# Kernel optimization log

Measured on AMD Instinct MI355X. Metric: run time of the kernel, lower is better.

Reference implementation:

```python
import jax, jax.numpy as jnp
import numpy as np

D_MODEL = 1024
N_HEADS = 16
DH = D_MODEL // N_HEADS
ROPE_THETA = 10000.0


def rotate_half(u):
    h = u.shape[-1] // 2
    return jnp.concatenate([-u[..., h:], u[..., :h]], axis=-1)


def apply_rope(q, k, cos, sin):
    return q * cos + rotate_half(q) * sin, k * cos + rotate_half(k) * sin


def setup_inputs() -> dict:
    key = jax.random.key(0)
    ks = jax.random.split(key, 6)
    B, S = 2, 2048
    x = jax.random.normal(ks[0], (B, S, D_MODEL), dtype=jnp.float32)
    y = jax.random.normal(ks[1], (B, S, D_MODEL), dtype=jnp.float32)
    wq = 0.01 * jax.random.normal(ks[2], (D_MODEL, D_MODEL), dtype=jnp.float32)
    wk = 0.01 * jax.random.normal(ks[3], (D_MODEL, D_MODEL), dtype=jnp.float32)
    wv = 0.01 * jax.random.normal(ks[4], (D_MODEL, D_MODEL), dtype=jnp.float32)
    wo = 0.01 * jax.random.normal(ks[5], (D_MODEL, D_MODEL), dtype=jnp.float32)
    return {"x": x, "y": y, "wq": wq, "wk": wk, "wv": wv, "wo": wo}


def reference(x, y, wq, wk, wv, wo):
    B, S, D = x.shape
    past_length = 0  # default; kv_cache=None

    Q = x @ wq.T                      # (B,S,D)
    K = y                             # NOTE: K is y un-projected (as in source)
    V = y @ wv.T
    # K1 = x @ wk.T is computed in the source but immediately overwritten
    # by the buggy second apply_rope call -> wk is unused in the output.
    V1 = x @ wo.T

    def heads(t):
        return t.reshape(B, S, N_HEADS, DH).transpose(0, 2, 1, 3)  # (B,H,S,dh)

    q_h, k_h, v_h, v1_h = heads(Q), heads(K), heads(V), heads(V1)

    # RoPE tables (past_length:past_length+S rows of the cache)
    freqs = 1.0 / ROPE_THETA ** (jnp.arange(0, DH, 2, dtype=jnp.float32) / DH)
    emb = jnp.arange(past_length, past_length + S, dtype=jnp.float32)[:, None] * freqs[None, :]
    cos = jnp.concatenate([jnp.cos(emb), jnp.cos(emb)], axis=-1)[None, None]  # (1,1,S,dh)
    sin = jnp.concatenate([jnp.sin(emb), jnp.sin(emb)], axis=-1)[None, None]

    q_h, k_h = apply_rope(q_h, k_h, cos, sin)
    # faithful to source: k1 = rope applied AGAIN to the already-roped k
    _, k1_h = apply_rope(q_h, k_h, cos, sin)

    k_full = jnp.concatenate([k_h, k1_h], axis=2)   # (B,H,2S,dh)
    v_full = jnp.concatenate([v_h, v1_h], axis=2)
    S_full = k_full.shape[2]

    # mask: tril(diagonal=past_length) over (S,S_full), last S cols = eye(S)
    rows = jnp.arange(S)[:, None]
    cols = jnp.arange(S_full)[None, :]
    mask = cols <= rows + past_length
    mask = mask.at[:, -S:].set(jnp.eye(S, dtype=bool))  # (S,S_full)

    scores = jnp.einsum("bhqd,bhkd->bhqk", q_h, k_full) / jnp.sqrt(jnp.asarray(DH, x.dtype))
    scores = jnp.where(mask[None, None], scores, jnp.asarray(-1e30, x.dtype))
    attn = jax.nn.softmax(scores, axis=-1)
    out = jnp.einsum("bhqk,bhkd->bhqd", attn, v_full)
    out = out.transpose(0, 2, 1, 3).reshape(B, S, D)

    k_ret = k_full[:, :, :-S, :]
    return out, k_ret
```

## Files before the change

kernel.cpp:

```cpp
#include <hip/hip_runtime.h>

#define DM 1024
#define NHEADS 16
#define DHEAD 64
#define BB 2
#define SS 2048
#define BH (BB*NHEADS)

typedef __attribute__((ext_vector_type(8))) short short8;
typedef __attribute__((ext_vector_type(4))) float float4v;
typedef unsigned short ushort_t;

#define LN1E4_D32 0.28782313662425572f

static __device__ __forceinline__ unsigned short f2bf(float f) {
    union { float f; unsigned u; } v; v.f = f;
    unsigned r = v.u + 0x7fffu + ((v.u >> 16) & 1u);
    return (unsigned short)(r >> 16);
}
static __device__ __forceinline__ float bf2f(unsigned short u) {
    union { float f; unsigned u; } v; v.u = ((unsigned)u) << 16;
    return v.f;
}

static __device__ __forceinline__ void gload16(const ushort_t* g, ushort_t* l) {
    __builtin_amdgcn_global_load_lds(
        (const __attribute__((address_space(1))) void*)g,
        (__attribute__((address_space(3))) void*)l, 16, 0, 0);
}

__global__ __launch_bounds__(256) void cvt_tile_kernel(
        const float* __restrict__ x, const float* __restrict__ wq,
        const float* __restrict__ wv, const float* __restrict__ wo,
        ushort_t* __restrict__ xb, ushort_t* __restrict__ wqb,
        ushort_t* __restrict__ wvb, ushort_t* __restrict__ wob) {
    int C = blockIdx.x * 256 + threadIdx.x;
    int c  = C & 511;
    int tl = C >> 9;
    int rb = tl >> 5, kb = tl & 31;
    const float* src; ushort_t* dst; int r0;
    if (rb < 32)      { src = x;  r0 = rb * 128;        dst = xb  + (size_t)tl * 4096; }
    else if (rb < 40) { src = wq; r0 = (rb - 32) * 128; dst = wqb + (size_t)(((rb - 32) * 32) + kb) * 4096; }
    else if (rb < 48) { src = wv; r0 = (rb - 40) * 128; dst = wvb + (size_t)(((rb - 40) * 32) + kb) * 4096; }
    else              { src = wo; r0 = (rb - 48) * 128; dst = wob + (size_t)(((rb - 48) * 32) + kb) * 4096; }
    int row = c >> 2, g = c & 3;
    int kk3 = g ^ ((row >> 1) & 3);
    const float* s = src + (size_t)(r0 + row) * DM + kb * 32 + kk3 * 8;
    float4 a0 = *reinterpret_cast<const float4*>(s);
    float4 a1 = *reinterpret_cast<const float4*>(s + 4);
    short8 v;
    v[0] = (short)f2bf(a0.x); v[1] = (short)f2bf(a0.y);
    v[2] = (short)f2bf(a0.z); v[3] = (short)f2bf(a0.w);
    v[4] = (short)f2bf(a1.x); v[5] = (short)f2bf(a1.y);
    v[6] = (short)f2bf(a1.z); v[7] = (short)f2bf(a1.w);
    *reinterpret_cast<short8*>(dst + c * 8) = v;
}

__global__ __launch_bounds__(256) void rope_k_kernel(const float* __restrict__ y,
        float* __restrict__ kout, ushort_t* __restrict__ khb, ushort_t* __restrict__ yb) {
    int t = blockIdx.x * blockDim.x + threadIdx.x;
    int i8 = t & 3;
    int s  = (t >> 2) & (SS - 1);
    int bh = t >> 13;
    int h = bh & (NHEADS - 1), b = bh >> 4;

    const float* yp = y + ((size_t)(b * SS + s)) * DM + h * DHEAD + i8 * 8;
    float4 a0 = *reinterpret_cast<const float4*>(yp);
    float4 a1 = *reinterpret_cast<const float4*>(yp + 4);
    float4 b0 = *reinterpret_cast<const float4*>(yp + 32);
    float4 b1 = *reinterpret_cast<const float4*>(yp + 36);
    float u0[8] = {a0.x, a0.y, a0.z, a0.w, a1.x, a1.y, a1.z, a1.w};
    float u1[8] = {b0.x, b0.y, b0.z, b0.w, b1.x, b1.y, b1.z, b1.w};
    float lo[8], hi[8];
#pragma unroll
    for (int j = 0; j < 8; j++) {
        int i = i8 * 8 + j;
        float freq = __expf(-(float)i * LN1E4_D32);
        float th = (float)s * freq;
        float cv = cosf(th), sv = sinf(th);
        lo[j] = u0[j] * cv - u1[j] * sv;
        hi[j] = u1[j] * cv + u0[j] * sv;
    }
    float* op = kout + ((size_t)bh * SS + s) * DHEAD + i8 * 8;
    *reinterpret_cast<float4*>(op)      = (float4){lo[0], lo[1], lo[2], lo[3]};
    *reinterpret_cast<float4*>(op + 4)  = (float4){lo[4], lo[5], lo[6], lo[7]};
    *reinterpret_cast<float4*>(op + 32) = (float4){hi[0], hi[1], hi[2], hi[3]};
    *reinterpret_cast<float4*>(op + 36) = (float4){hi[4], hi[5], hi[6], hi[7]};

    ushort_t* kb = khb + ((size_t)bh * 32 + (s >> 6)) * 4096 + (s & 63) * 64;
    short8 vlo, vhi;
#pragma unroll
    for (int j = 0; j < 8; j++) { vlo[j] = (short)f2bf(lo[j]); vhi[j] = (short)f2bf(hi[j]); }
    *reinterpret_cast<short8*>(kb + ((i8 ^ (s & 7)) << 3))       = vlo;
    *reinterpret_cast<short8*>(kb + (((i8 + 4) ^ (s & 7)) << 3)) = vhi;

    int rowm = b * SS + s;
    int rowin = rowm & 127, rbm = rowm >> 7;
    int g = i8 ^ ((rowin >> 1) & 3);
    ushort_t* yt = yb + ((size_t)(rbm * 32 + h * 2)) * 4096 + rowin * 32 + (g << 3);
    short8 ulo, uhi;
#pragma unroll
    for (int j = 0; j < 8; j++) { ulo[j] = (short)f2bf(u0[j]); uhi[j] = (short)f2bf(u1[j]); }
    *reinterpret_cast<short8*>(yt)        = ulo;
    *reinterpret_cast<short8*>(yt + 4096) = uhi;
}

__global__ __launch_bounds__(256, 2) void gemm3_kernel(
        const ushort_t* __restrict__ xb, const ushort_t* __restrict__ yb,
        const ushort_t* __restrict__ wqb, const ushort_t* __restrict__ wvb,
        const ushort_t* __restrict__ wob,
        ushort_t* __restrict__ qh, ushort_t* __restrict__ vt, ushort_t* __restrict__ v1h) {
    __shared__ __align__(16) char smem[34816];
    ushort_t* As = (ushort_t*)smem;
    ushort_t* Bs = (ushort_t*)(smem + 16384);
    ushort_t (*Ct)[136] = (ushort_t(*)[136])smem;

    int bid = blockIdx.x;
    int xcd = bid & 7;
    int s_  = bid >> 3;
    int zo  = s_ >> 5;
    int z   = (zo == 0) ? 0 : (zo == 1 ? 2 : 1);
    int t_  = s_ & 31;
    int n0  = (t_ >> 2) * 128;
    int m0  = (xcd * 4 + (t_ & 3)) * 128;

    const ushort_t* A = (z == 1) ? yb : xb;
    const ushort_t* W = (z == 0) ? wqb : (z == 1 ? wvb : wob);
    ushort_t* O = (z == 0) ? qh : (z == 1 ? vt : v1h);

    const ushort_t* Atl = A + (size_t)(m0 >> 7) * 32 * 4096;
    const ushort_t* Wtl = W + (size_t)(n0 >> 7) * 32 * 4096;

    int tid = threadIdx.x;
    int wave = tid >> 6, lane = tid & 63, quad = lane >> 4, l15 = lane & 15;
    int wr = (wave >> 1) * 64, wc = (wave & 1) * 64;

    int gi0 = tid * 8, gi1 = (256 + tid) * 8;
    int li0 = (tid & 192) * 8, li1 = (256 + (tid & 192)) * 8;

    int aoff[4], boff[4];
#pragma unroll
    for (int mi = 0; mi < 4; mi++) {
        int row = wr + mi * 16 + l15;
        aoff[mi] = row * 32 + ((quad ^ ((row >> 1) & 3)) << 3);
    }
#pragma unroll
    for (int ni = 0; ni < 4; ni++) {
        int row = wc + ni * 16 + l15;
        boff[ni] = row * 32 + ((quad ^ ((row >> 1) & 3)) << 3);
    }

    float4v acc[4][4];
#pragma unroll
    for (int a = 0; a < 4; a++)
#pragma unroll
        for (int b = 0; b < 4; b++)
            acc[a][b] = (float4v){0.f, 0.f, 0.f, 0.f};

    gload16(Atl + gi0, As + li0); gload16(Atl + gi1, As + li1);
    gload16(Wtl + gi0, Bs + li0); gload16(Wtl + gi1, Bs + li1);
    int cur = 0;

    for (int kb = 0; kb < 32; kb++) {
        __syncthreads();
        if (kb + 1 < 32) {
            const ushort_t* at = Atl + (size_t)(kb + 1) * 4096;
            const ushort_t* wt = Wtl + (size_t)(kb + 1) * 4096;
            int nb = (cur ^ 1) * 4096;
            gload16(at + gi0, As + nb + li0); gload16(at + gi1, As + nb + li1);
            gload16(wt + gi0, Bs + nb + li0); gload16(wt + gi1, Bs + nb + li1);
        }
        const ushort_t* Ac = As + cur * 4096;
        const ushort_t* Bc = Bs + cur * 4096;
        short8 af[4], bfr[4];
#pragma unroll
        for (int mi = 0; mi < 4; mi++)
            af[mi] = *reinterpret_cast<const short8*>(&Ac[aoff[mi]]);
#pragma unroll
        for (int ni = 0; ni < 4; ni++)
            bfr[ni] = *reinterpret_cast<const short8*>(&Bc[boff[ni]]);
#pragma unroll
        for (int mi = 0; mi < 4; mi++)
#pragma unroll
            for (int ni = 0; ni < 4; ni++)
                acc[mi][ni] = __builtin_amdgcn_mfma_f32_16x16x32_bf16(af[mi], bfr[ni], acc[mi][ni], 0, 0, 0);
        cur ^= 1;
    }

    if (z == 0) {
#pragma unroll
        for (int mi = 0; mi < 4; mi++)
#pragma unroll
            for (int r = 0; r < 4; r++) {
                int m = m0 + wr + mi * 16 + quad * 4 + r;
                float pos = (float)(m & (SS - 1));
#pragma unroll
                for (int ni = 0; ni < 2; ni++) {
                    int d = ni * 16 + l15;
                    float f = __expf(-(float)d * LN1E4_D32);
                    float th = pos * f;
                    float cv, sv;
                    __sincosf(th, &sv, &cv);
                    float u0 = acc[mi][ni][r], u1 = acc[mi][ni + 2][r];
                    acc[mi][ni][r]     = u0 * cv - u1 * sv;
                    acc[mi][ni + 2][r] = u1 * cv + u0 * sv;
                }
            }
    }

    __syncthreads();
#pragma unroll
    for (int mi = 0; mi < 4; mi++)
#pragma unroll
        for (int ni = 0; ni < 4; ni++) {
            int col = wc + ni * 16 + l15;
#pragma unroll
            for (int r = 0; r < 4; r++)
                Ct[wr + mi * 16 + quad * 4 + r][col] = f2bf(acc[mi][ni][r]);
        }
    __syncthreads();
    int h0 = n0 >> 6;
    if (z == 1) {
        int b = m0 >> 11;
        int s0 = m0 & (SS - 1);
#pragma unroll
        for (int it = 0; it < 8; it++) {
            int c = it * 256 + tid;
            int dh  = c & 63;
            int k16 = (c >> 6) & 15;
            int hh  = c >> 10;
            short8 v;
#pragma unroll
            for (int e = 0; e < 8; e++)
                v[e] = (short)Ct[k16 * 8 + e][hh * 64 + dh];
            int kt = (s0 >> 6) + (k16 >> 3);
            size_t off = ((size_t)((b * NHEADS + h0 + hh) * 32 + kt)) * 4096
                       + dh * 64 + (((k16 & 7) ^ (dh & 7)) << 3);
            *reinterpret_cast<short8*>(&O[off]) = v;
        }
    } else {
#pragma unroll
        for (int it = 0; it < 8; it++) {
            int c = it * 256 + tid;
            int o = c >> 3, j = c & 7;
            int hh = o >> 7, mr = o & 127;
            int m = m0 + mr, b = m >> 11, si = m & (SS - 1);
            uint4 v = *reinterpret_cast<const uint4*>(&Ct[mr][hh * 64 + j * 8]);
            *reinterpret_cast<uint4*>(
                &O[((size_t)((b * NHEADS + h0 + hh) * SS + si)) * DHEAD + j * 8]) = v;
        }
    }
}

__global__ __launch_bounds__(256, 2) void attn_kernel(
        const ushort_t* __restrict__ qh, const float* __restrict__ kf32,
        const ushort_t* __restrict__ khb, const ushort_t* __restrict__ vtb,
        const ushort_t* __restrict__ v1h, float* __restrict__ out) {
    __shared__ __align__(16) ushort_t Ks[2][4096];
    __shared__ __align__(16) ushort_t Vt[2][4096];
    __shared__ ushort_t Ps[4][16][68];
    __shared__ float sdiag[4][16];

    int bid = blockIdx.x;
    int bh = (bid & 7) * 4 + ((bid >> 3) & 3);
    int qb = 31 - (bid >> 5);
    int q0 = qb * 64;

    int tid = threadIdx.x, wave = tid >> 6, lane = tid & 63, quad = lane >> 4, l15 = lane & 15;
    int q0w = q0 + wave * 16;
    const ushort_t* qp  = qh  + (size_t)bh * SS * DHEAD;
    const float*    kp  = kf32 + (size_t)bh * SS * DHEAD;
    const ushort_t* v1p = v1h + (size_t)bh * SS * DHEAD;
    const ushort_t* ktb = khb + (size_t)bh * 32 * 4096;
    const ushort_t* vtt = vtb + (size_t)bh * 32 * 4096;

    short8 qf[2];
    qf[0] = *reinterpret_cast<const short8*>(&qp[(q0w + l15) * DHEAD + quad * 8]);
    qf[1] = *reinterpret_cast<const short8*>(&qp[(q0w + l15) * DHEAD + 32 + quad * 8]);

    float4v Oa[4];
#pragma unroll
    for (int t = 0; t < 4; t++) Oa[t] = (float4v){0.f, 0.f, 0.f, 0.f};
    float lsum[4] = {0.f, 0.f, 0.f, 0.f};

    int gi0 = tid * 8, gi1 = (256 + tid) * 8;
    int li0 = (tid & 192) * 8, li1 = (256 + (tid & 192)) * 8;

    int ntiles = qb + 1;
    gload16(ktb + gi0, &Ks[0][li0]); gload16(ktb + gi1, &Ks[0][li1]);
    gload16(vtt + gi0, &Vt[0][li0]); gload16(vtt + gi1, &Vt[0][li1]);
    int cur = 0;

    for (int kt = 0; kt < ntiles; kt++) {
        __syncthreads();
        if (kt + 1 < ntiles) {
            const ushort_t* gk = ktb + (size_t)(kt + 1) * 4096;
            const ushort_t* gv = vtt + (size_t)(kt + 1) * 4096;
            int nb = cur ^ 1;
            gload16(gk + gi0, &Ks[nb][li0]); gload16(gk + gi1, &Ks[nb][li1]);
            gload16(gv + gi0, &Vt[nb][li0]); gload16(gv + gi1, &Vt[nb][li1]);
        }
        const ushort_t* Kc = Ks[cur];
        const ushort_t* Vc = Vt[cur];

        float4v sa[4];
#pragma unroll
        for (int t2 = 0; t2 < 4; t2++) sa[t2] = (float4v){0.f, 0.f, 0.f, 0.f};
#pragma unroll
        for (int t2 = 0; t2 < 4; t2++) {
            int key = t2 * 16 + l15;
            int ro = key * 64, sw = key & 7;
#pragma unroll
            for (int half = 0; half < 2; half++) {
                short8 kf = *reinterpret_cast<const short8*>(&Kc[ro + (((half * 4 + quad) ^ sw) << 3)]);
                sa[t2] = __builtin_amdgcn_mfma_f32_16x16x32_bf16(qf[half], kf, sa[t2], 0, 0, 0);
            }
        }

        int kbase = kt * 64;
#pragma unroll
        for (int r = 0; r < 4; r++) {
            int query = q0w + quad * 4 + r;
#pragma unroll
            for (int t2 = 0; t2 < 4; t2++) {
                int key = kbase + t2 * 16 + l15;
                float p = (key <= query) ? __expf(sa[t2][r] * 0.125f) : 0.f;
                Ps[wave][quad * 4 + r][t2 * 16 + l15] = f2bf(p);
                lsum[r] += p;
            }
        }
        short8 pf0 = *reinterpret_cast<const short8*>(&Ps[wave][l15][quad * 8]);
        short8 pf1 = *reinterpret_cast<const short8*>(&Ps[wave][l15][32 + quad * 8]);
#pragma unroll
        for (int t = 0; t < 4; t++) {
            int dh = t * 16 + l15;
            int ro = dh * 64, sw = dh & 7;
            short8 vf0 = *reinterpret_cast<const short8*>(&Vc[ro + ((quad ^ sw) << 3)]);
            short8 vf1 = *reinterpret_cast<const short8*>(&Vc[ro + (((4 + quad) ^ sw) << 3)]);
            Oa[t] = __builtin_amdgcn_mfma_f32_16x16x32_bf16(pf0, vf0, Oa[t], 0, 0, 0);
            Oa[t] = __builtin_amdgcn_mfma_f32_16x16x32_bf16(pf1, vf1, Oa[t], 0, 0, 0);
        }
        cur ^= 1;
    }

    {
        int sk = q0w + l15;
        const float* krow = kp + (size_t)sk * DHEAD;
        short8 k1lo, k1hi;
#pragma unroll
        for (int j = 0; j < 8; j++) {
            int d = quad * 8 + j;
            float f = __expf(-(float)d * LN1E4_D32);
            float th = (float)sk * f;
            float cv, sv;
            __sincosf(th, &sv, &cv);
            float a = krow[d], b2 = krow[d + 32];
            k1lo[j] = (short)f2bf(a * cv - b2 * sv);
            k1hi[j] = (short)f2bf(b2 * cv + a * sv);
        }
        float4v sd4 = (float4v){0.f, 0.f, 0.f, 0.f};
        sd4 = __builtin_amdgcn_mfma_f32_16x16x32_bf16(qf[0], k1lo, sd4, 0, 0, 0);
        sd4 = __builtin_amdgcn_mfma_f32_16x16x32_bf16(qf[1], k1hi, sd4, 0, 0, 0);
#pragma unroll
        for (int r = 0; r < 4; r++)
            if (l15 == quad * 4 + r) sdiag[wave][l15] = sd4[r] * 0.125f;
        __syncthreads();

        int b = bh >> 4, h = bh & (NHEADS - 1);
#pragma unroll
        for (int r = 0; r < 4; r++) {
            float ls = lsum[r];
#pragma unroll
            for (int off = 1; off < 16; off <<= 1) ls += __shfl_xor(ls, off);
            float pd = __expf(sdiag[wave][quad * 4 + r]);
            int query = q0w + quad * 4 + r;
            float linv = 1.f / (ls + pd);
#pragma unroll
            for (int t = 0; t < 4; t++) {
                float v1v = bf2f(v1p[query * DHEAD + t * 16 + l15]);
                float o = (Oa[t][r] + pd * v1v) * linv;
                out[(b * SS + query) * DM + h * DHEAD + t * 16 + l15] = o;
            }
        }
    }
}

extern "C" void kernel_launch(void* const* d_in, const int* in_sizes, int n_in,
                              void* d_out, int out_size, void* d_ws, size_t ws_size,
                              hipStream_t stream) {
    const float* x  = (const float*)d_in[0];
    const float* y  = (const float*)d_in[1];
    const float* wq = (const float*)d_in[2];
    const float* wv = (const float*)d_in[4];
    const float* wo = (const float*)d_in[5];
    float* outp  = (float*)d_out;
    float* k_out = outp + (size_t)BB * SS * DM;

    char* ws = (char*)d_ws;
    ushort_t* vtb = (ushort_t*)(ws);
    ushort_t* v1b = (ushort_t*)(ws + (8ull  << 20));
    ushort_t* qhb = (ushort_t*)(ws + (16ull << 20));
    ushort_t* khb = (ushort_t*)(ws + (24ull << 20));
    ushort_t* xb  = (ushort_t*)(ws + (32ull << 20));
    ushort_t* yb  = (ushort_t*)(ws + (40ull << 20));
    ushort_t* wqb = (ushort_t*)(ws + (48ull << 20));
    ushort_t* wvb = (ushort_t*)(ws + (50ull << 20));
    ushort_t* wob = (ushort_t*)(ws + (52ull << 20));

    cvt_tile_kernel<<<3584, 256, 0, stream>>>(x, wq, wv, wo, xb, wqb, wvb, wob);
    rope_k_kernel<<<1024, 256, 0, stream>>>(y, k_out, khb, yb);
    gemm3_kernel<<<768, 256, 0, stream>>>(xb, yb, wqb, wvb, wob, qhb, vtb, v1b);
    attn_kernel<<<1024, 256, 0, stream>>>(qhb, k_out, khb, vtb, v1b, outp);
}
```

Before: 184.6 us.

## Peel masked diagonal tile and transpose QK MFMA for packed P stores

Splits the key loop so all off-diagonal tiles run a mask-free path and only the final diagonal tile applies the causal mask. It also swaps the MFMA operand order so each lane holds four consecutive keys for one query, which allows packed bf16 conversion and 32-bit stores into the P scratch (padded to 70). The row-sum reduction becomes two cross-quad shuffles plus a shared-memory exchange instead of per-row 16-lane butterflies. The intent is to cut VALU and LDS work in the inner loop, at the cost of an extra shared array and using inline assembly for the conversion.

```diff
diff --git a/kernel.cpp b/kernel.cpp
--- a/kernel.cpp
+++ b/kernel.cpp
@@ -21,6 +21,11 @@
 static __device__ __forceinline__ float bf2f(unsigned short u) {
     union { float f; unsigned u; } v; v.u = ((unsigned)u) << 16;
     return v.f;
+}
+static __device__ __forceinline__ unsigned cvtpk_bf16(float lo, float hi) {
+    unsigned r;
+    asm("v_cvt_pk_bf16_f32 %0, %1, %2" : "=v"(r) : "v"(lo), "v"(hi));
+    return r;
 }
 
 static __device__ __forceinline__ void gload16(const ushort_t* g, ushort_t* l) {
@@ -252,14 +257,66 @@
     }
 }
 
+template<bool MASKED>
+static __device__ __forceinline__ void attn_tile(
+        const ushort_t* __restrict__ Kc, const ushort_t* __restrict__ Vc, int kbase,
+        int quad, int l15, int q0w, const short8* qf,
+        ushort_t (*Psw)[70], float4v* Oa, float& lsum) {
+    float4v sa[4];
+#pragma unroll
+    for (int t2 = 0; t2 < 4; t2++) sa[t2] = (float4v){0.f, 0.f, 0.f, 0.f};
+#pragma unroll
+    for (int t2 = 0; t2 < 4; t2++) {
+        int key = t2 * 16 + l15;
+        int ro = key * 64, sw = key & 7;
+#pragma unroll
+        for (int half = 0; half < 2; half++) {
+            short8 kf = *reinterpret_cast<const short8*>(&Kc[ro + (((half * 4 + quad) ^ sw) << 3)]);
+            sa[t2] = __builtin_amdgcn_mfma_f32_16x16x32_bf16(kf, qf[half], sa[t2], 0, 0, 0);
+        }
+    }
+    int query = q0w + l15;
+#pragma unroll
+    for (int t2 = 0; t2 < 4; t2++) {
+        float p[4];
+#pragma unroll
+        for (int r = 0; r < 4; r++) {
+            float e = __expf(sa[t2][r] * 0.125f);
+            if (MASKED) {
+                int key = kbase + t2 * 16 + quad * 4 + r;
+                p[r] = (key <= query) ? e : 0.f;
+            } else {
+                p[r] = e;
+            }
+        }
+        lsum += (p[0] + p[1]) + (p[2] + p[3]);
+        unsigned w0 = cvtpk_bf16(p[0], p[1]);
+        unsigned w1 = cvtpk_bf16(p[2], p[3]);
+        *reinterpret_cast<unsigned*>(&Psw[l15][t2 * 16 + quad * 4])     = w0;
+        *reinterpret_cast<unsigned*>(&Psw[l15][t2 * 16 + quad * 4 + 2]) = w1;
+    }
+    short8 pf0 = *reinterpret_cast<const short8*>(&Psw[l15][quad * 8]);
+    short8 pf1 = *reinterpret_cast<const short8*>(&Psw[l15][32 + quad * 8]);
+#pragma unroll
+    for (int t = 0; t < 4; t++) {
+        int dh = t * 16 + l15;
+        int ro = dh * 64, sw = dh & 7;
+        short8 vf0 = *reinterpret_cast<const short8*>(&Vc[ro + ((quad ^ sw) << 3)]);
+        short8 vf1 = *reinterpret_cast<const short8*>(&Vc[ro + (((4 + quad) ^ sw) << 3)]);
+        Oa[t] = __builtin_amdgcn_mfma_f32_16x16x32_bf16(pf0, vf0, Oa[t], 0, 0, 0);
+        Oa[t] = __builtin_amdgcn_mfma_f32_16x16x32_bf16(pf1, vf1, Oa[t], 0, 0, 0);
+    }
+}
+
 __global__ __launch_bounds__(256, 2) void attn_kernel(
         const ushort_t* __restrict__ qh, const float* __restrict__ kf32,
         const ushort_t* __restrict__ khb, const ushort_t* __restrict__ vtb,
         const ushort_t* __restrict__ v1h, float* __restrict__ out) {
     __shared__ __align__(16) ushort_t Ks[2][4096];
     __shared__ __align__(16) ushort_t Vt[2][4096];
-    __shared__ ushort_t Ps[4][16][68];
+    __shared__ ushort_t Ps[4][16][70];
     __shared__ float sdiag[4][16];
+    __shared__ float sred[4][16];
 
     int bid = blockIdx.x;
     int bh = (bid & 7) * 4 + ((bid >> 3) & 3);
@@ -281,67 +338,31 @@
     float4v Oa[4];
 #pragma unroll
     for (int t = 0; t < 4; t++) Oa[t] = (float4v){0.f, 0.f, 0.f, 0.f};
-    float lsum[4] = {0.f, 0.f, 0.f, 0.f};
+    float lsum = 0.f;
 
     int gi0 = tid * 8, gi1 = (256 + tid) * 8;
     int li0 = (tid & 192) * 8, li1 = (256 + (tid & 192)) * 8;
 
-    int ntiles = qb + 1;
     gload16(ktb + gi0, &Ks[0][li0]); gload16(ktb + gi1, &Ks[0][li1]);
     gload16(vtt + gi0, &Vt[0][li0]); gload16(vtt + gi1, &Vt[0][li1]);
     int cur = 0;
 
-    for (int kt = 0; kt < ntiles; kt++) {
+    for (int kt = 0; kt < qb; kt++) {
         __syncthreads();
-        if (kt + 1 < ntiles) {
-            const ushort_t* gk = ktb + (size_t)(kt + 1) * 4096;
-            const ushort_t* gv = vtt + (size_t)(kt + 1) * 4096;
-            int nb = cur ^ 1;
-            gload16(gk + gi0, &Ks[nb][li0]); gload16(gk + gi1, &Ks[nb][li1]);
-            gload16(gv + gi0, &Vt[nb][li0]); gload16(gv + gi1, &Vt[nb][li1]);
-        }
-        const ushort_t* Kc = Ks[cur];
-        const ushort_t* Vc = Vt[cur];
-
-        float4v sa[4];
-#pragma unroll
-        for (int t2 = 0; t2 < 4; t2++) sa[t2] = (float4v){0.f, 0.f, 0.f, 0.f};
-#pragma unroll
-        for (int t2 = 0; t2 < 4; t2++) {
-            int key = t2 * 16 + l15;
-            int ro = key * 64, sw = key & 7;
-#pragma unroll
-            for (int half = 0; half < 2; half++) {
-                short8 kf = *reinterpret_cast<const short8*>(&Kc[ro + (((half * 4 + quad) ^ sw) << 3)]);
-                sa[t2] = __builtin_amdgcn_mfma_f32_16x16x32_bf16(qf[half], kf, sa[t2], 0, 0, 0);
-            }
-        }
-
-        int kbase = kt * 64;
-#pragma unroll
-        for (int r = 0; r < 4; r++) {
-            int query = q0w + quad * 4 + r;
-#pragma unroll
-            for (int t2 = 0; t2 < 4; t2++) {
-                int key = kbase + t2 * 16 + l15;
-                float p = (key <= query) ? __expf(sa[t2][r] * 0.125f) : 0.f;
-                Ps[wave][quad * 4 + r][t2 * 16 + l15] = f2bf(p);
-                lsum[r] += p;
-            }
-        }
-        short8 pf0 = *reinterpret_cast<const short8*>(&Ps[wave][l15][quad * 8]);
-        short8 pf1 = *reinterpret_cast<const short8*>(&Ps[wave][l15][32 + quad * 8]);
-#pragma unroll
-        for (int t = 0; t < 4; t++) {
-            int dh = t * 16 + l15;
-            int ro = dh * 64, sw = dh & 7;
-            short8 vf0 = *reinterpret_cast<const short8*>(&Vc[ro + ((quad ^ sw) << 3)]);
-            short8 vf1 = *reinterpret_cast<const short8*>(&Vc[ro + (((4 + quad) ^ sw) << 3)]);
-            Oa[t] = __builtin_amdgcn_mfma_f32_16x16x32_bf16(pf0, vf0, Oa[t], 0, 0, 0);
-            Oa[t] = __builtin_amdgcn_mfma_f32_16x16x32_bf16(pf1, vf1, Oa[t], 0, 0, 0);
-        }
+        const ushort_t* gk = ktb + (size_t)(kt + 1) * 4096;
+        const ushort_t* gv = vtt + (size_t)(kt + 1) * 4096;
+        int nb = cur ^ 1;
+        gload16(gk + gi0, &Ks[nb][li0]); gload16(gk + gi1, &Ks[nb][li1]);
+        gload16(gv + gi0, &Vt[nb][li0]); gload16(gv + gi1, &Vt[nb][li1]);
+        attn_tile<false>(Ks[cur], Vt[cur], kt * 64, quad, l15, q0w, qf, Ps[wave], Oa, lsum);
         cur ^= 1;
     }
+    __syncthreads();
+    attn_tile<true>(Ks[cur], Vt[cur], qb * 64, quad, l15, q0w, qf, Ps[wave], Oa, lsum);
+
+    lsum += __shfl_xor(lsum, 16);
+    lsum += __shfl_xor(lsum, 32);
+    if (quad == 0) sred[wave][l15] = lsum;
 
     {
         int sk = q0w + l15;
@@ -369,9 +390,7 @@
         int b = bh >> 4, h = bh & (NHEADS - 1);
 #pragma unroll
         for (int r = 0; r < 4; r++) {
-            float ls = lsum[r];
-#pragma unroll
-            for (int off = 1; off < 16; off <<= 1) ls += __shfl_xor(ls, off);
+            float ls = sred[wave][quad * 4 + r];
             float pd = __expf(sdiag[wave][quad * 4 + r]);
             int query = q0w + quad * 4 + r;
             float linv = 1.f / (ls + pd);
```

Result: faster. 176.1 us (-4.6%).
